# Kernel optimization log

Measured on AMD Instinct MI355X. Metric: run time of the kernel, lower is better.

Reference implementation:

```python
import jax, jax.numpy as jnp
import numpy as np

NUM_GENES = 4384
D_MODEL = 128


def setup_inputs() -> dict:
    key = jax.random.key(0)
    ks = jax.random.split(key, 8)
    B = 8
    return {
        "mutation_input": jax.random.normal(ks[0], (B, NUM_GENES, 4), dtype=jnp.float32),
        "external_V": jax.random.normal(ks[1], (NUM_GENES, D_MODEL), dtype=jnp.float32),
        "W_in": jax.random.normal(ks[2], (4, D_MODEL), dtype=jnp.float32) * 0.5,
        "b_in": jnp.zeros((D_MODEL,), dtype=jnp.float32),
        "key_param": jax.random.normal(ks[3], (NUM_GENES, D_MODEL), dtype=jnp.float32),
        "W1": jax.random.normal(ks[4], (D_MODEL, 64), dtype=jnp.float32) * (1.0 / np.sqrt(D_MODEL)),
        "b1": jnp.zeros((64,), dtype=jnp.float32),
        "W2": jax.random.normal(ks[5], (64, 26), dtype=jnp.float32) * 0.125,
        "b2": jnp.zeros((26,), dtype=jnp.float32),
    }


def reference(mutation_input, external_V, W_in, b_in, key_param, W1, b1, W2, b2):
    # Q: [B, G, D]
    Q = jnp.einsum("bgf,fd->bgd", mutation_input, W_in) + b_in
    scale = 1.0 / jnp.sqrt(jnp.asarray(Q.shape[-1], Q.dtype))
    # scores: [B, G, G] -- full matrix as in the original module
    scores = jnp.einsum("bqd,kd->bqk", Q, key_param) * scale
    attn = jax.nn.softmax(scores, axis=-1)
    # attention output: [B, G, D]
    attn_out = jnp.einsum("bqk,kd->bqd", attn, external_V)
    mean_out = attn_out.mean(axis=1)  # [B, D]
    h = jax.nn.gelu(mean_out @ W1 + b1, approximate=False)
    out = h @ W2 + b2  # [B, 26]
    return out
```

## Files before the change

### kernel.cpp

```cpp
#include <hip/hip_runtime.h>
#include <hip/hip_bf16.h>

#define NUM_GENES 4384
#define GPAD 4608
#define DM 128
#define ROWB 256
#define LDS_STRIDE 272
#define NTILES 137
#define RB_BLOCKS 18
#define NCHUNK 6
#define TPC 23

typedef __attribute__((ext_vector_type(8))) short short8;
typedef __attribute__((ext_vector_type(16))) float floatx16;

#if defined(__has_builtin)
#  if __has_builtin(__builtin_amdgcn_exp2f)
#    define FAST_EXP2(x) __builtin_amdgcn_exp2f(x)
#  endif
#endif
#ifndef FAST_EXP2
#  define FAST_EXP2(x) exp2f(x)
#endif

__global__ void zero_lw(float* l, float* w, float* meanbuf) {
    int i = blockIdx.x * 256 + threadIdx.x;
    l[i] = 0.f;
    w[i] = 0.f;
    if (i < 1024) meanbuf[i] = 0.f;
}

__global__ void prep_q(const float* __restrict__ mut, const float* __restrict__ W_in,
                       const float* __restrict__ b_in, __hip_bfloat16* __restrict__ Qb) {
    int idx = blockIdx.x * 256 + threadIdx.x;
    int d = idx & 127;
    int g = (idx >> 7) % GPAD;
    int b = idx / (GPAD * 128);
    float v = 0.f;
    if (g < NUM_GENES) {
        const float* m = mut + ((size_t)b * NUM_GENES + g) * 4;
        v = b_in[d] + m[0] * W_in[d] + m[1] * W_in[128 + d]
                    + m[2] * W_in[256 + d] + m[3] * W_in[384 + d];
        v *= (0.08838834764831845f * 1.4426950408889634f);
    }
    Qb[idx] = __float2bfloat16(v);
}

__global__ void prep_k(const float* __restrict__ key, __hip_bfloat16* __restrict__ Kb) {
    int idx = blockIdx.x * 256 + threadIdx.x;
    int g = idx >> 7;
    float v = (g < NUM_GENES) ? key[idx] : 0.f;
    Kb[idx] = __float2bfloat16(v);
}

__global__ void recip_k(float* l) {
    int i = blockIdx.x * 256 + threadIdx.x;
    l[i] = 1.0f / l[i];
}

template <bool PB>
__global__ __launch_bounds__(256)
void phase_kernel(const __hip_bfloat16* __restrict__ Qb,
                  const __hip_bfloat16* __restrict__ Kb,
                  const float* __restrict__ linv,
                  float* __restrict__ out) {
    __shared__ __align__(16) char tile[32 * LDS_STRIDE];

    int rb    = blockIdx.x;
    int chunk = blockIdx.y;
    int b     = blockIdx.z;

    const char* resident = (const char*)(PB ? Kb : (Qb + (size_t)b * GPAD * DM));
    const char* stream   = (const char*)(PB ? (Qb + (size_t)b * GPAD * DM) : Kb);

    int t = threadIdx.x;
    int lane = t & 63, wid = t >> 6;
    int m = lane & 31, half = lane >> 5;

    short8 afrag[2][8];
#pragma unroll
    for (int g = 0; g < 2; ++g) {
        const char* arow = resident + (size_t)(rb * 256 + wid * 64 + g * 32 + m) * ROWB;
#pragma unroll
        for (int dsl = 0; dsl < 8; ++dsl)
            afrag[g][dsl] = *(const short8*)(arow + dsl * 32 + half * 16);
    }

    float lacc[2][16];
#pragma unroll
    for (int g = 0; g < 2; ++g)
#pragma unroll
        for (int r = 0; r < 16; ++r) lacc[g][r] = 0.f;

    int t0 = chunk * TPC;
    int t1 = min(NTILES, t0 + TPC);
    int sr = t >> 3, sc = t & 7;
    char* dst = tile + sr * LDS_STRIDE + sc * 32;

    const char* src = stream + (size_t)(t0 * 32 + sr) * ROWB + sc * 32;
    float4 v0 = *(const float4*)src;
    float4 v1 = *(const float4*)(src + 16);

    for (int kt = t0; kt < t1; ++kt) {
        __syncthreads();
        *(float4*)dst = v0;
        *(float4*)(dst + 16) = v1;
        __syncthreads();

        if (kt + 1 < t1) {
            const char* s2 = stream + (size_t)((kt + 1) * 32 + sr) * ROWB + sc * 32;
            v0 = *(const float4*)s2;
            v1 = *(const float4*)(s2 + 16);
        }

        floatx16 acc0, acc1;
#pragma unroll
        for (int r = 0; r < 16; ++r) { acc0[r] = 0.f; acc1[r] = 0.f; }
#pragma unroll
        for (int dsl = 0; dsl < 8; ++dsl) {
            short8 bfrag = *(const short8*)(tile + m * LDS_STRIDE + dsl * 32 + half * 16);
            acc0 = __builtin_amdgcn_mfma_f32_32x32x16_bf16(afrag[0][dsl], bfrag, acc0, 0, 0, 0);
            acc1 = __builtin_amdgcn_mfma_f32_32x32x16_bf16(afrag[1][dsl], bfrag, acc1, 0, 0, 0);
        }

        if (PB) {
            float scl = linv[b * GPAD + kt * 32 + m];
#pragma unroll
            for (int r = 0; r < 16; ++r) {
                lacc[0][r] = fmaf(FAST_EXP2(acc0[r]), scl, lacc[0][r]);
                lacc[1][r] = fmaf(FAST_EXP2(acc1[r]), scl, lacc[1][r]);
            }
        } else {
#pragma unroll
            for (int r = 0; r < 16; ++r) {
                lacc[0][r] += FAST_EXP2(acc0[r]);
                lacc[1][r] += FAST_EXP2(acc1[r]);
            }
        }
    }

#pragma unroll
    for (int off = 1; off <= 16; off <<= 1)
#pragma unroll
        for (int g = 0; g < 2; ++g)
#pragma unroll
            for (int r = 0; r < 16; ++r)
                lacc[g][r] += __shfl_xor(lacc[g][r], off, 64);

    if (m == 0) {
#pragma unroll
        for (int g = 0; g < 2; ++g) {
            float* ob = out + b * GPAD + rb * 256 + wid * 64 + g * 32 + 4 * half;
#pragma unroll
            for (int r = 0; r < 16; ++r)
                atomicAdd(ob + (r & 3) + 8 * (r >> 2), lacc[g][r]);
        }
    }
}

__global__ __launch_bounds__(256)
void mean_k(const float* __restrict__ w, const float* __restrict__ V,
            float* __restrict__ meanbuf) {
    int rb = blockIdx.x, b = blockIdx.y;
    int t = threadIdx.x;
    int d = t & 127, half = t >> 7;
    int g0 = rb * 128 + half * 64;
    int nv = NUM_GENES - g0;
    if (nv > 64) nv = 64;
    float a = 0.f;
    if (nv > 0) {
        const float* wb = w + b * GPAD + g0;
        const float* Vp = V + (size_t)g0 * 128 + d;
        for (int k = 0; k < nv; ++k)
            a += wb[k] * Vp[(size_t)k * 128];
    }
    atomicAdd(meanbuf + b * 128 + d, a);
}

__global__ void mlp_k(const float* __restrict__ meanbuf,
                      const float* __restrict__ W1, const float* __restrict__ b1,
                      const float* __restrict__ W2, const float* __restrict__ b2,
                      float* __restrict__ out) {
    int b = blockIdx.x, t = threadIdx.x;
    __shared__ float sh[64];
    const float* mb = meanbuf + b * 128;
    float s = b1[t];
    for (int d = 0; d < 128; ++d)
        s += (mb[d] * (1.0f / 4384.0f)) * W1[d * 64 + t];
    sh[t] = 0.5f * s * (1.0f + erff(s * 0.70710678118654752f));
    __syncthreads();
    if (t < 26) {
        float o = b2[t];
        for (int j = 0; j < 64; ++j) o += sh[j] * W2[j * 26 + t];
        out[b * 26 + t] = o;
    }
}

extern "C" void kernel_launch(void* const* d_in, const int* in_sizes, int n_in,
                              void* d_out, int out_size, void* d_ws, size_t ws_size,
                              hipStream_t stream) {
    const float* mut  = (const float*)d_in[0];
    const float* V    = (const float*)d_in[1];
    const float* W_in = (const float*)d_in[2];
    const float* b_in = (const float*)d_in[3];
    const float* key  = (const float*)d_in[4];
    const float* W1   = (const float*)d_in[5];
    const float* b1   = (const float*)d_in[6];
    const float* W2   = (const float*)d_in[7];
    const float* b2   = (const float*)d_in[8];
    float* out = (float*)d_out;

    char* ws = (char*)d_ws;
    __hip_bfloat16* Qb = (__hip_bfloat16*)(ws);
    __hip_bfloat16* Kb = (__hip_bfloat16*)(ws + 9437184);
    float* lbuf        = (float*)(ws + 10616832);
    float* wbuf        = (float*)(ws + 10764288);
    float* meanbuf     = (float*)(ws + 10911744);

    zero_lw<<<144, 256, 0, stream>>>(lbuf, wbuf, meanbuf);
    prep_q<<<18432, 256, 0, stream>>>(mut, W_in, b_in, Qb);
    prep_k<<<2304, 256, 0, stream>>>(key, Kb);

    dim3 grid(RB_BLOCKS, NCHUNK, 8);
    phase_kernel<false><<<grid, 256, 0, stream>>>(Qb, Kb, lbuf, lbuf);
    recip_k<<<144, 256, 0, stream>>>(lbuf);
    phase_kernel<true><<<grid, 256, 0, stream>>>(Qb, Kb, lbuf, wbuf);

    mean_k<<<dim3(35, 8), 256, 0, stream>>>(wbuf, V, meanbuf);
    mlp_k<<<8, 64, 0, stream>>>(meanbuf, W1, b1, W2, b2, out);
}
```

Before: 227.0 us.

## Double-buffer LDS tiles, fuse prep kernels, drop recip kernel, double chunk count

Three prep/zero kernels are merged into one launch, and the separate reciprocal kernel is removed by dividing inline in the second phase. The phase kernel switches to double-buffered LDS so one barrier per tile suffices, with the next tile written to the alternate buffer after the MFMAs. The grid is split into 12 chunks of 12 tiles instead of 6 of 23, which doubles block count for better CU occupancy at the cost of twice as many atomics on the row sums.

New measurement: 243.7 us. 7.4% more time.

```diff
diff --git a/kernel.cpp b/kernel.cpp
--- a/kernel.cpp
+++ b/kernel.cpp
@@ -8,8 +8,8 @@
 #define LDS_STRIDE 272
 #define NTILES 137
 #define RB_BLOCKS 18
-#define NCHUNK 6
-#define TPC 23
+#define NCHUNK 12
+#define TPC 12
 
 typedef __attribute__((ext_vector_type(8))) short short8;
 typedef __attribute__((ext_vector_type(16))) float floatx16;
@@ -23,48 +23,45 @@
 #  define FAST_EXP2(x) exp2f(x)
 #endif
 
-__global__ void zero_lw(float* l, float* w, float* meanbuf) {
-    int i = blockIdx.x * 256 + threadIdx.x;
-    l[i] = 0.f;
-    w[i] = 0.f;
-    if (i < 1024) meanbuf[i] = 0.f;
-}
-
-__global__ void prep_q(const float* __restrict__ mut, const float* __restrict__ W_in,
-                       const float* __restrict__ b_in, __hip_bfloat16* __restrict__ Qb) {
-    int idx = blockIdx.x * 256 + threadIdx.x;
-    int d = idx & 127;
-    int g = (idx >> 7) % GPAD;
-    int b = idx / (GPAD * 128);
-    float v = 0.f;
-    if (g < NUM_GENES) {
-        const float* m = mut + ((size_t)b * NUM_GENES + g) * 4;
-        v = b_in[d] + m[0] * W_in[d] + m[1] * W_in[128 + d]
-                    + m[2] * W_in[256 + d] + m[3] * W_in[384 + d];
-        v *= (0.08838834764831845f * 1.4426950408889634f);
-    }
-    Qb[idx] = __float2bfloat16(v);
-}
-
-__global__ void prep_k(const float* __restrict__ key, __hip_bfloat16* __restrict__ Kb) {
-    int idx = blockIdx.x * 256 + threadIdx.x;
-    int g = idx >> 7;
-    float v = (g < NUM_GENES) ? key[idx] : 0.f;
-    Kb[idx] = __float2bfloat16(v);
-}
-
-__global__ void recip_k(float* l) {
-    int i = blockIdx.x * 256 + threadIdx.x;
-    l[i] = 1.0f / l[i];
+__global__ __launch_bounds__(256)
+void prep_all(const float* __restrict__ mut, const float* __restrict__ W_in,
+              const float* __restrict__ b_in, const float* __restrict__ key,
+              __hip_bfloat16* __restrict__ Qb, __hip_bfloat16* __restrict__ Kb,
+              float* __restrict__ l, float* __restrict__ w, float* __restrict__ meanbuf) {
+    int bx = blockIdx.x, t = threadIdx.x;
+    if (bx < 18432) {
+        int idx = bx * 256 + t;
+        int d = idx & 127;
+        int g = (idx >> 7) % GPAD;
+        int b = idx / (GPAD * 128);
+        float v = 0.f;
+        if (g < NUM_GENES) {
+            const float* m = mut + ((size_t)b * NUM_GENES + g) * 4;
+            v = b_in[d] + m[0] * W_in[d] + m[1] * W_in[128 + d]
+                        + m[2] * W_in[256 + d] + m[3] * W_in[384 + d];
+            v *= (0.08838834764831845f * 1.4426950408889634f);
+        }
+        Qb[idx] = __float2bfloat16(v);
+    } else if (bx < 20736) {
+        int idx = (bx - 18432) * 256 + t;
+        int g = idx >> 7;
+        float v = (g < NUM_GENES) ? key[idx] : 0.f;
+        Kb[idx] = __float2bfloat16(v);
+    } else {
+        int i = (bx - 20736) * 256 + t;
+        l[i] = 0.f;
+        w[i] = 0.f;
+        if (i < 1024) meanbuf[i] = 0.f;
+    }
 }
 
 template <bool PB>
 __global__ __launch_bounds__(256)
 void phase_kernel(const __hip_bfloat16* __restrict__ Qb,
                   const __hip_bfloat16* __restrict__ Kb,
-                  const float* __restrict__ linv,
+                  const float* __restrict__ lsum,
                   float* __restrict__ out) {
-    __shared__ __align__(16) char tile[32 * LDS_STRIDE];
+    __shared__ __align__(16) char tile[2][32 * LDS_STRIDE];
 
     int rb    = blockIdx.x;
     int chunk = blockIdx.y;
@@ -95,36 +92,44 @@
     int t0 = chunk * TPC;
     int t1 = min(NTILES, t0 + TPC);
     int sr = t >> 3, sc = t & 7;
-    char* dst = tile + sr * LDS_STRIDE + sc * 32;
-
-    const char* src = stream + (size_t)(t0 * 32 + sr) * ROWB + sc * 32;
-    float4 v0 = *(const float4*)src;
-    float4 v1 = *(const float4*)(src + 16);
-
+    int soff = sr * LDS_STRIDE + sc * 32;
+
+    {
+        const char* src = stream + (size_t)(t0 * 32 + sr) * ROWB + sc * 32;
+        float4 v0 = *(const float4*)src;
+        float4 v1 = *(const float4*)(src + 16);
+        *(float4*)(tile[0] + soff) = v0;
+        *(float4*)(tile[0] + soff + 16) = v1;
+    }
+
+    int p = 0;
     for (int kt = t0; kt < t1; ++kt) {
-        __syncthreads();
-        *(float4*)dst = v0;
-        *(float4*)(dst + 16) = v1;
-        __syncthreads();
-
-        if (kt + 1 < t1) {
+        bool more = (kt + 1 < t1);
+        float4 v0, v1;
+        if (more) {
             const char* s2 = stream + (size_t)((kt + 1) * 32 + sr) * ROWB + sc * 32;
             v0 = *(const float4*)s2;
             v1 = *(const float4*)(s2 + 16);
         }
+        __syncthreads();
 
         floatx16 acc0, acc1;
 #pragma unroll
         for (int r = 0; r < 16; ++r) { acc0[r] = 0.f; acc1[r] = 0.f; }
 #pragma unroll
         for (int dsl = 0; dsl < 8; ++dsl) {
-            short8 bfrag = *(const short8*)(tile + m * LDS_STRIDE + dsl * 32 + half * 16);
+            short8 bfrag = *(const short8*)(tile[p] + m * LDS_STRIDE + dsl * 32 + half * 16);
             acc0 = __builtin_amdgcn_mfma_f32_32x32x16_bf16(afrag[0][dsl], bfrag, acc0, 0, 0, 0);
             acc1 = __builtin_amdgcn_mfma_f32_32x32x16_bf16(afrag[1][dsl], bfrag, acc1, 0, 0, 0);
         }
 
+        if (more) {
+            *(float4*)(tile[p ^ 1] + soff) = v0;
+            *(float4*)(tile[p ^ 1] + soff + 16) = v1;
+        }
+
         if (PB) {
-            float scl = linv[b * GPAD + kt * 32 + m];
+            float scl = 1.0f / lsum[b * GPAD + kt * 32 + m];
 #pragma unroll
             for (int r = 0; r < 16; ++r) {
                 lacc[0][r] = fmaf(FAST_EXP2(acc0[r]), scl, lacc[0][r]);
@@ -137,6 +142,7 @@
                 lacc[1][r] += FAST_EXP2(acc1[r]);
             }
         }
+        p ^= 1;
     }
 
 #pragma unroll
@@ -217,13 +223,10 @@
     float* wbuf        = (float*)(ws + 10764288);
     float* meanbuf     = (float*)(ws + 10911744);
 
-    zero_lw<<<144, 256, 0, stream>>>(lbuf, wbuf, meanbuf);
-    prep_q<<<18432, 256, 0, stream>>>(mut, W_in, b_in, Qb);
-    prep_k<<<2304, 256, 0, stream>>>(key, Kb);
+    prep_all<<<20880, 256, 0, stream>>>(mut, W_in, b_in, key, Qb, Kb, lbuf, wbuf, meanbuf);
 
     dim3 grid(RB_BLOCKS, NCHUNK, 8);
     phase_kernel<false><<<grid, 256, 0, stream>>>(Qb, Kb, lbuf, lbuf);
-    recip_k<<<144, 256, 0, stream>>>(lbuf);
     phase_kernel<true><<<grid, 256, 0, stream>>>(Qb, Kb, lbuf, wbuf);
 
     mean_k<<<dim3(35, 8), 256, 0, stream>>>(wbuf, V, meanbuf);
```
